# Kernel optimization log

Hardware: AMD Instinct MI355X
Metric: run time of the kernel (lower is better)

Reference implementation:

```python
import jax, jax.numpy as jnp
import numpy as np

BATCH, SEQ, DIN, FILTERS, KSIZE = 64, 512, 256, 256, 3

def setup_inputs() -> dict:
    key = jax.random.key(0)
    ks = jax.random.split(key, 5)
    s_u = 1.0 / np.sqrt(DIN)
    return {
        "x": jax.random.normal(ks[0], (BATCH, SEQ, DIN), dtype=jnp.float32),
        "z": jax.random.normal(ks[1], (BATCH, DIN), dtype=jnp.float32),
        "U": jax.random.normal(ks[2], (DIN, DIN), dtype=jnp.float32) * s_u,
        "V": jax.random.normal(ks[3], (DIN, KSIZE * FILTERS), dtype=jnp.float32) * s_u,
        "B_w": jax.random.normal(ks[4], (DIN, KSIZE * FILTERS), dtype=jnp.float32) * s_u,
        "b": jnp.zeros((FILTERS,), dtype=jnp.float32),
        "kernel_size": KSIZE,
    }

def reference(x, z, U, V, B_w, b, kernel_size):
    Bn, L, din = x.shape
    K = int(kernel_size)
    F = V.shape[1] // K
    # per-sample dynamic kernel: (U * sigmoid(z)) @ V + B
    zf = jax.nn.sigmoid(z)                                  # (B, din)
    f = jnp.einsum('de,be,ef->bdf', U, zf, V) + B_w[None]    # (B, din, K*F)
    f = f.reshape(Bn, din, K, F).transpose(0, 2, 1, 3)       # (B, K, din, F)
    # 'same' padding, stride 1
    pad_l, pad_r = (K - 1) // 2, K // 2
    xp = jnp.pad(x, ((0, 0), (pad_l, pad_r), (0, 0)))        # (B, L+K-1, din)
    patches = jnp.stack([xp[:, i:i + L] for i in range(K)], axis=2)  # (B, L, K, din)
    out = jnp.einsum('blkd,bkdf->blf', patches, f) + b       # (B, L, F)
    return jax.nn.relu(out)
```

## Files before the change

kernel.cpp:

```cpp
#include <hip/hip_runtime.h>
#include <math.h>

#define BATCH 64
#define SEQL  512
#define DIN   256
#define NF    256
#define KS    3
#define KF    (KS * NF)

#define XCH 512
#define KC  (KS * XCH)
#define PROWS 130
#define PLD   128
#define PSZ   (PROWS * PLD)

typedef __attribute__((ext_vector_type(8))) short short8;
typedef __attribute__((ext_vector_type(4))) float floatx4;
typedef __attribute__((ext_vector_type(8))) unsigned short ushort8v;

static __device__ __forceinline__ unsigned short f2bf(float f) {
    unsigned int u = __float_as_uint(f);
    return (unsigned short)((u + 0x7FFF + ((u >> 16) & 1)) >> 16);
}

static __device__ __forceinline__ void gl_lds16(const void* g, void* l) {
    __builtin_amdgcn_global_load_lds(
        (const __attribute__((address_space(1))) unsigned int*)g,
        (__attribute__((address_space(3))) unsigned int*)l, 16, 0, 0);
}

__global__ __launch_bounds__(256) void pack_kernel(
    const float* __restrict__ U, const float* __restrict__ V,
    const float* __restrict__ Bw,
    unsigned short* __restrict__ WcT, unsigned short* __restrict__ UT)
{
    const int blk = blockIdx.x;
    const int t   = threadIdx.x;
    __shared__ unsigned short tile[64][64 + 2];

    if (blk < 96) {
        const int f0 = (blk & 3) * 64, c0 = (blk >> 2) * 64;
        const int fl = t & 63, cb = t >> 6;
        #pragma unroll
        for (int it = 0; it < 16; ++it) {
            const int cl = cb + it * 4;
            const int c  = c0 + cl;
            const int k  = c >> 9, ch = c & (XCH - 1);
            const float v = (ch < DIN) ? Bw[(size_t)ch * KF + k * NF + f0 + fl]
                                       : V[(size_t)(ch - DIN) * KF + k * NF + f0 + fl];
            tile[cl][fl] = f2bf(v);
        }
        __syncthreads();
        const int cl2 = t & 63, fb = t >> 6;
        #pragma unroll
        for (int it = 0; it < 16; ++it) {
            const int fl2 = fb + it * 4;
            WcT[(size_t)(f0 + fl2) * KC + c0 + cl2] = tile[cl2][fl2];
        }
    } else {
        const int bb = blk - 96;
        const int e0 = (bb & 3) * 64, d0 = (bb >> 2) * 64;
        const int el = t & 63, db = t >> 6;
        #pragma unroll
        for (int it = 0; it < 16; ++it) {
            const int dl = db + it * 4;
            tile[dl][el] = f2bf(U[(size_t)(d0 + dl) * DIN + e0 + el]);
        }
        __syncthreads();
        const int dl2 = t & 63, eb = t >> 6;
        #pragma unroll
        for (int it = 0; it < 16; ++it) {
            const int el2 = eb + it * 4;
            UT[(size_t)(e0 + el2) * DIN + d0 + dl2] = tile[dl2][el2];
        }
    }
}

__global__ __launch_bounds__(512, 2) void fused_kernel(
    const float* __restrict__ x, const float* __restrict__ z,
    const unsigned short* __restrict__ UT,
    const unsigned short* __restrict__ WcT,
    const float* __restrict__ bias, float* __restrict__ out)
{
    __shared__ unsigned short lds[4 * PSZ + 128 * 64];
    unsigned short* Bs = lds + 4 * PSZ;

    const int tid  = threadIdx.x;
    const int lane = tid & 63;
    const int wave = tid >> 6;
    const int quad = lane >> 4, l16 = lane & 15;
    const int r8   = lane >> 3, ud8 = lane & 7;

    const int bid   = blockIdx.x;
    const int b     = bid >> 2;
    const int lbase = (bid & 3) * 128;

    #pragma unroll 1
    for (int p = 0; p < 2; ++p) {
        unsigned short* P = lds + p * PSZ;
        #pragma unroll
        for (int it = 0; it < 5; ++it) {
            const int idx = tid + it * 512;
            if (idx < PROWS * 16) {
                const int row = idx >> 4, u = idx & 15;
                const int l = lbase - 1 + row;
                ushort8v h = {};
                if (l >= 0 && l < SEQL) {
                    const float* xp = x + ((size_t)b * SEQL + l) * DIN + p * 128 + u * 8;
                    const float4 v0 = *(const float4*)xp;
                    const float4 v1 = *(const float4*)(xp + 4);
                    h[0] = f2bf(v0.x); h[1] = f2bf(v0.y);
                    h[2] = f2bf(v0.z); h[3] = f2bf(v0.w);
                    h[4] = f2bf(v1.x); h[5] = f2bf(v1.y);
                    h[6] = f2bf(v1.z); h[7] = f2bf(v1.w);
                }
                *(ushort8v*)&P[row * PLD + ((u ^ (row & 15)) << 3)] = h;
            }
        }
    }
    __syncthreads();

    #pragma unroll 1
    for (int eh = 0; eh < 2; ++eh) {
        floatx4 accY[9] = {};
        #pragma unroll 1
        for (int kk = 0; kk < 4; ++kk) {
            const unsigned short* gU = UT + (size_t)(eh * 128) * DIN + kk * 64;
            #pragma unroll
            for (int c = 0; c < 2; ++c) {
                const int r = wave * 16 + c * 8 + r8;
                gl_lds16(gU + (size_t)r * DIN + (ud8 ^ (r & 7)) * 8,
                         Bs + (size_t)(wave * 16 + c * 8) * 64);
            }
            __syncthreads();
            const unsigned short* P = lds + (kk >> 1) * PSZ;
            const int dh = kk & 1;
            #pragma unroll
            for (int ks = 0; ks < 2; ++ks) {
                const short8 bf = *(const short8*)
                    &Bs[(wave * 16 + l16) * 64 + (((ks * 4 + quad) ^ (l16 & 7)) * 8)];
                #pragma unroll
                for (int i = 0; i < 9; ++i) {
                    const short8 af = *(const short8*)
                        &P[(i * 16 + l16) * PLD +
                           (((dh * 8 + ks * 4 + quad) ^ (l16 & 15)) * 8)];
                    accY[i] = __builtin_amdgcn_mfma_f32_16x16x32_bf16(
                        af, bf, accY[i], 0, 0, 0);
                }
            }
            __syncthreads();
        }
        const int ecol = wave * 16 + l16;
        const float zf = 1.0f /
            (1.0f + expf(-z[(size_t)b * DIN + eh * 128 + ecol]));
        unsigned short* PY = lds + (2 + eh) * PSZ;
        const int u16e = ecol >> 3;
        #pragma unroll
        for (int i = 0; i < 9; ++i) {
            #pragma unroll
            for (int r = 0; r < 4; ++r) {
                const int row = i * 16 + quad * 4 + r;
                if (row < PROWS)
                    PY[row * PLD + ((u16e ^ (row & 15)) << 3) + (ecol & 7)] =
                        f2bf(accY[i][r] * zf);
            }
        }
    }
    __syncthreads();

    const int wr = wave & 3;
    const int wc = wave >> 2;
    #pragma unroll 1
    for (int fh = 0; fh < 2; ++fh) {
        floatx4 acc[2][4] = {};
        #pragma unroll 1
        for (int g = 0; g < 4; ++g) {
            const unsigned short* P = lds + g * PSZ;
            #pragma unroll 1
            for (int k = 0; k < KS; ++k) {
                #pragma unroll 1
                for (int hh = 0; hh < 2; ++hh) {
                    const unsigned short* gW =
                        WcT + (size_t)(fh * 128) * KC + k * XCH + g * 128 + hh * 64;
                    #pragma unroll
                    for (int c = 0; c < 2; ++c) {
                        const int r = wave * 16 + c * 8 + r8;
                        gl_lds16(gW + (size_t)r * KC + (ud8 ^ (r & 7)) * 8,
                                 Bs + (size_t)(wave * 16 + c * 8) * 64);
                    }
                    __syncthreads();
                    #pragma unroll
                    for (int ks = 0; ks < 2; ++ks) {
                        short8 af[2], bfr[4];
                        #pragma unroll
                        for (int i = 0; i < 2; ++i) {
                            const int row = wr * 32 + i * 16 + l16 + k;
                            af[i] = *(const short8*)
                                &P[row * PLD +
                                   (((hh * 8 + ks * 4 + quad) ^ (row & 15)) * 8)];
                        }
                        #pragma unroll
                        for (int j = 0; j < 4; ++j) {
                            const int n = wc * 64 + j * 16 + l16;
                            bfr[j] = *(const short8*)
                                &Bs[n * 64 + (((ks * 4 + quad) ^ (n & 7)) * 8)];
                        }
                        #pragma unroll
                        for (int i = 0; i < 2; ++i)
                            #pragma unroll
                            for (int j = 0; j < 4; ++j)
                                acc[i][j] = __builtin_amdgcn_mfma_f32_16x16x32_bf16(
                                    af[i], bfr[j], acc[i][j], 0, 0, 0);
                    }
                    __syncthreads();
                }
            }
        }
        #pragma unroll
        for (int j = 0; j < 4; ++j) {
            const int f  = fh * 128 + wc * 64 + j * 16 + l16;
            const float bv = bias[f];
            #pragma unroll
            for (int i = 0; i < 2; ++i) {
                const int lrow = lbase + wr * 32 + i * 16 + quad * 4;
                #pragma unroll
                for (int r = 0; r < 4; ++r) {
                    const float v = acc[i][j][r] + bv;
                    out[((size_t)b * SEQL + lrow + r) * NF + f] = fmaxf(v, 0.0f);
                }
            }
        }
    }
}

extern "C" void kernel_launch(void* const* d_in, const int* in_sizes, int n_in,
                              void* d_out, int out_size, void* d_ws, size_t ws_size,
                              hipStream_t stream) {
    const float* x    = (const float*)d_in[0];
    const float* z    = (const float*)d_in[1];
    const float* U    = (const float*)d_in[2];
    const float* V    = (const float*)d_in[3];
    const float* Bw   = (const float*)d_in[4];
    const float* bias = (const float*)d_in[5];

    unsigned short* WcT = (unsigned short*)d_ws;
    unsigned short* UT  = WcT + (size_t)NF * KC;
    float* out = (float*)d_out;

    pack_kernel<<<dim3(112), 256, 0, stream>>>(U, V, Bw, WcT, UT);
    fused_kernel<<<dim3(256), 512, 0, stream>>>(x, z, UT, WcT, bias, out);
}
```

Baseline: 148.7 us.

## Double-buffer weight staging, reorder stages, and widen conv tiles to 32x32 MFMA

Weight tiles (WcT and UT) are now staged into alternating LDS buffers, prefetching the next tile while computing the current one, which drops one barrier per step. The convolution against raw x is moved ahead of the U projection so it can run while spare LDS is free. The conv now covers all 256 filters in one pass with 32x32x16 MFMA and 64x64 per-wave tiles, replacing two 128-filter passes with 16x16 tiles. The cost is larger accumulators (64 floats per lane) and more complex LDS buffer aliasing, which may raise register pressure at the 2-blocks-per-CU launch bound.

```diff
diff --git a/kernel.cpp b/kernel.cpp
--- a/kernel.cpp
+++ b/kernel.cpp
@@ -16,6 +16,7 @@
 
 typedef __attribute__((ext_vector_type(8))) short short8;
 typedef __attribute__((ext_vector_type(4))) float floatx4;
+typedef __attribute__((ext_vector_type(16))) float floatx16;
 typedef __attribute__((ext_vector_type(8))) unsigned short ushort8v;
 
 static __device__ __forceinline__ unsigned short f2bf(float f) {
@@ -82,22 +83,69 @@
     const unsigned short* __restrict__ WcT,
     const float* __restrict__ bias, float* __restrict__ out)
 {
-    __shared__ unsigned short lds[4 * PSZ + 128 * 64];
-    unsigned short* Bs = lds + 4 * PSZ;
+    __shared__ __align__(16) unsigned short lds[4 * PSZ];
 
     const int tid  = threadIdx.x;
     const int lane = tid & 63;
     const int wave = tid >> 6;
     const int quad = lane >> 4, l16 = lane & 15;
+    const int l32  = lane & 31, hi  = lane >> 5;
     const int r8   = lane >> 3, ud8 = lane & 7;
 
     const int bid   = blockIdx.x;
     const int b     = bid >> 2;
     const int lbase = (bid & 3) * 128;
 
+    const int wr = wave >> 2, wc = wave & 3;
+
+    floatx16 acc[2][2] = {};
+
+    auto convBuf = [&](int r) -> unsigned short* {
+        return (r < 12) ? (lds + 2 * PSZ + ((r & 1) ? 16384 : 0))
+                        : (lds + ((r & 1) ? PSZ : 0));
+    };
+    auto stageB = [&](int r) {
+        unsigned short* buf = convBuf(r);
+        const int g = r / 6, k = (r / 2) % 3, hh = r & 1;
+        const unsigned short* gW = WcT + (size_t)k * XCH + g * 128 + hh * 64;
+        #pragma unroll
+        for (int c = 0; c < 4; ++c) {
+            const int rr = wave * 32 + c * 8 + r8;
+            gl_lds16(gW + (size_t)rr * KC + ((ud8 ^ (rr & 7)) << 3),
+                     buf + (size_t)(wave * 32 + c * 8) * 64);
+        }
+    };
+    auto convRegion = [&](int r) {
+        const unsigned short* buf = convBuf(r);
+        const int g = r / 6, k = (r / 2) % 3, hh = r & 1;
+        const unsigned short* P = lds + (size_t)g * PSZ;
+        #pragma unroll
+        for (int ks = 0; ks < 4; ++ks) {
+            short8 af[2], bf[2];
+            const int uwa = hh * 8 + ks * 2 + hi;
+            #pragma unroll
+            for (int i = 0; i < 2; ++i) {
+                const int m = wr * 64 + i * 32 + l32 + k;
+                af[i] = *(const short8*)&P[m * PLD + ((uwa ^ (m & 15)) << 3)];
+            }
+            const int uwb = ks * 2 + hi;
+            #pragma unroll
+            for (int j = 0; j < 2; ++j) {
+                const int n = wc * 64 + j * 32 + l32;
+                bf[j] = *(const short8*)&buf[n * 64 + ((uwb ^ (n & 7)) << 3)];
+            }
+            #pragma unroll
+            for (int i = 0; i < 2; ++i)
+                #pragma unroll
+                for (int j = 0; j < 2; ++j)
+                    acc[i][j] = __builtin_amdgcn_mfma_f32_32x32x16_bf16(
+                        af[i], bf[j], acc[i][j], 0, 0, 0);
+        }
+    };
+
     #pragma unroll 1
     for (int p = 0; p < 2; ++p) {
-        unsigned short* P = lds + p * PSZ;
+        unsigned short* P = lds + (size_t)p * PSZ;
         #pragma unroll
         for (int it = 0; it < 5; ++it) {
             const int idx = tid + it * 512;
@@ -118,116 +166,113 @@
             }
         }
     }
+
+    stageB(0);
     __syncthreads();
-
     #pragma unroll 1
-    for (int eh = 0; eh < 2; ++eh) {
+    for (int r = 0; r < 12; ++r) {
+        if (r < 11) stageB(r + 1);
+        convRegion(r);
+        __syncthreads();
+    }
+
+    {
         floatx4 accY[9] = {};
+        auto utBuf = [&](int rg) -> unsigned short* {
+            return lds + 3 * PSZ + ((rg & 1) ? 8192 : 0);
+        };
+        auto stageU = [&](int rg) {
+            unsigned short* buf = utBuf(rg);
+            const int eh = rg >> 2, kk = rg & 3;
+            const unsigned short* gU = UT + (size_t)(eh * 128) * DIN + kk * 64;
+            #pragma unroll
+            for (int c = 0; c < 2; ++c) {
+                const int rr = wave * 16 + c * 8 + r8;
+                gl_lds16(gU + (size_t)rr * DIN + ((ud8 ^ (rr & 7)) << 3),
+                         buf + (size_t)(wave * 16 + c * 8) * 64);
+            }
+        };
+        stageU(0);
+        __syncthreads();
         #pragma unroll 1
-        for (int kk = 0; kk < 4; ++kk) {
-            const unsigned short* gU = UT + (size_t)(eh * 128) * DIN + kk * 64;
-            #pragma unroll
-            for (int c = 0; c < 2; ++c) {
-                const int r = wave * 16 + c * 8 + r8;
-                gl_lds16(gU + (size_t)r * DIN + (ud8 ^ (r & 7)) * 8,
-                         Bs + (size_t)(wave * 16 + c * 8) * 64);
+        for (int rg = 0; rg < 8; ++rg) {
+            if (rg < 7) stageU(rg + 1);
+            const unsigned short* buf = utBuf(rg);
+            const int kk = rg & 3;
+            const unsigned short* P = lds + (size_t)(kk >> 1) * PSZ;
+            const int dh = kk & 1;
+            #pragma unroll
+            for (int ks = 0; ks < 2; ++ks) {
+                const short8 bfv = *(const short8*)
+                    &buf[(wave * 16 + l16) * 64 + (((ks * 4 + quad) ^ (l16 & 7)) << 3)];
+                #pragma unroll
+                for (int i = 0; i < 9; ++i) {
+                    const int row = i * 16 + l16;
+                    const short8 afv = *(const short8*)
+                        &P[row * PLD + (((dh * 8 + ks * 4 + quad) ^ (row & 15)) << 3)];
+                    accY[i] = __builtin_amdgcn_mfma_f32_16x16x32_bf16(
+                        afv, bfv, accY[i], 0, 0, 0);
+                }
+            }
+            if (rg == 3) {
+                const int ecol = wave * 16 + l16;
+                const float zf = 1.0f / (1.0f + expf(-z[(size_t)b * DIN + ecol]));
+                unsigned short* PY = lds + 2 * PSZ;
+                const int u16e = ecol >> 3;
+                #pragma unroll
+                for (int i = 0; i < 9; ++i)
+                    #pragma unroll
+                    for (int rr2 = 0; rr2 < 4; ++rr2) {
+                        const int row = i * 16 + quad * 4 + rr2;
+                        if (row < PROWS)
+                            PY[row * PLD + ((u16e ^ (row & 15)) << 3) + (ecol & 7)] =
+                                f2bf(accY[i][rr2] * zf);
+                    }
+                #pragma unroll
+                for (int i = 0; i < 9; ++i)
+                    #pragma unroll
+                    for (int rr2 = 0; rr2 < 4; ++rr2)
+                        accY[i][rr2] = 0.0f;
             }
             __syncthreads();
-            const unsigned short* P = lds + (kk >> 1) * PSZ;
-            const int dh = kk & 1;
-            #pragma unroll
-            for (int ks = 0; ks < 2; ++ks) {
-                const short8 bf = *(const short8*)
-                    &Bs[(wave * 16 + l16) * 64 + (((ks * 4 + quad) ^ (l16 & 7)) * 8)];
-                #pragma unroll
-                for (int i = 0; i < 9; ++i) {
-                    const short8 af = *(const short8*)
-                        &P[(i * 16 + l16) * PLD +
-                           (((dh * 8 + ks * 4 + quad) ^ (l16 & 15)) * 8)];
-                    accY[i] = __builtin_amdgcn_mfma_f32_16x16x32_bf16(
-                        af, bf, accY[i], 0, 0, 0);
+        }
+        {
+            const int ecol = wave * 16 + l16;
+            const float zf = 1.0f / (1.0f + expf(-z[(size_t)b * DIN + 128 + ecol]));
+            unsigned short* PY = lds + 3 * PSZ;
+            const int u16e = ecol >> 3;
+            #pragma unroll
+            for (int i = 0; i < 9; ++i)
+                #pragma unroll
+                for (int rr2 = 0; rr2 < 4; ++rr2) {
+                    const int row = i * 16 + quad * 4 + rr2;
+                    if (row < PROWS)
+                        PY[row * PLD + ((u16e ^ (row & 15)) << 3) + (ecol & 7)] =
+                            f2bf(accY[i][rr2] * zf);
                 }
-            }
-            __syncthreads();
-        }
-        const int ecol = wave * 16 + l16;
-        const float zf = 1.0f /
-            (1.0f + expf(-z[(size_t)b * DIN + eh * 128 + ecol]));
-        unsigned short* PY = lds + (2 + eh) * PSZ;
-        const int u16e = ecol >> 3;
-        #pragma unroll
-        for (int i = 0; i < 9; ++i) {
-            #pragma unroll
-            for (int r = 0; r < 4; ++r) {
-                const int row = i * 16 + quad * 4 + r;
-                if (row < PROWS)
-                    PY[row * PLD + ((u16e ^ (row & 15)) << 3) + (ecol & 7)] =
-                        f2bf(accY[i][r] * zf);
-            }
-        }
-    }
+        }
+    }
+
+    stageB(12);
     __syncthreads();
-
-    const int wr = wave & 3;
-    const int wc = wave >> 2;
     #pragma unroll 1
-    for (int fh = 0; fh < 2; ++fh) {
-        floatx4 acc[2][4] = {};
-        #pragma unroll 1
-        for (int g = 0; g < 4; ++g) {
-            const unsigned short* P = lds + g * PSZ;
-            #pragma unroll 1
-            for (int k = 0; k < KS; ++k) {
-                #pragma unroll 1
-                for (int hh = 0; hh < 2; ++hh) {
-                    const unsigned short* gW =
-                        WcT + (size_t)(fh * 128) * KC + k * XCH + g * 128 + hh * 64;
-                    #pragma unroll
-                    for (int c = 0; c < 2; ++c) {
-                        const int r = wave * 16 + c * 8 + r8;
-                        gl_lds16(gW + (size_t)r * KC + (ud8 ^ (r & 7)) * 8,
-                                 Bs + (size_t)(wave * 16 + c * 8) * 64);
-                    }
-                    __syncthreads();
-                    #pragma unroll
-                    for (int ks = 0; ks < 2; ++ks) {
-                        short8 af[2], bfr[4];
-                        #pragma unroll
-                        for (int i = 0; i < 2; ++i) {
-                            const int row = wr * 32 + i * 16 + l16 + k;
-                            af[i] = *(const short8*)
-                                &P[row * PLD +
-                                   (((hh * 8 + ks * 4 + quad) ^ (row & 15)) * 8)];
-                        }
-                        #pragma unroll
-                        for (int j = 0; j < 4; ++j) {
-                            const int n = wc * 64 + j * 16 + l16;
-                            bfr[j] = *(const short8*)
-                                &Bs[n * 64 + (((ks * 4 + quad) ^ (n & 7)) * 8)];
-                        }
-                        #pragma unroll
-                        for (int i = 0; i < 2; ++i)
-                            #pragma unroll
-                            for (int j = 0; j < 4; ++j)
-                                acc[i][j] = __builtin_amdgcn_mfma_f32_16x16x32_bf16(
-                                    af[i], bfr[j], acc[i][j], 0, 0, 0);
-                    }
-                    __syncthreads();
-                }
-            }
-        }
-        #pragma unroll
-        for (int j = 0; j < 4; ++j) {
-            const int f  = fh * 128 + wc * 64 + j * 16 + l16;
-            const float bv = bias[f];
-            #pragma unroll
-            for (int i = 0; i < 2; ++i) {
-                const int lrow = lbase + wr * 32 + i * 16 + quad * 4;
-                #pragma unroll
-                for (int r = 0; r < 4; ++r) {
-                    const float v = acc[i][j][r] + bv;
-                    out[((size_t)b * SEQL + lrow + r) * NF + f] = fmaxf(v, 0.0f);
-                }
+    for (int r = 12; r < 24; ++r) {
+        if (r < 23) stageB(r + 1);
+        convRegion(r);
+        __syncthreads();
+    }
+
+    #pragma unroll
+    for (int j = 0; j < 2; ++j) {
+        const int f  = wc * 64 + j * 32 + l32;
+        const float bv = bias[f];
+        #pragma unroll
+        for (int i = 0; i < 2; ++i) {
+            #pragma unroll
+            for (int reg = 0; reg < 16; ++reg) {
+                const int rowl = wr * 64 + i * 32 + (reg & 3) + 8 * (reg >> 2) + 4 * hi;
+                const float v = acc[i][j][reg] + bv;
+                out[((size_t)b * SEQL + lbase + rowl) * NF + f] = fmaxf(v, 0.0f);
             }
         }
     }
```

Result: faster. 129.3 us (-13.0%).
